# Kernel optimization log

Hardware: AMD Instinct MI355X
Metric: run time of the kernel (lower is better)

The kernel has to match this reference:

```python
import jax, jax.numpy as jnp
import numpy as np

D_MODEL, N_LEVELS, N_HEADS, N_POINTS = 256, 3, 8, 2
HEAD_DIM = D_MODEL // N_HEADS
SPATIAL_SHAPES = np.array([[100, 100], [50, 50], [25, 25]], dtype=np.int32)
LEN_IN = int((SPATIAL_SHAPES[:, 0] * SPATIAL_SHAPES[:, 1]).sum())  # 13125
BS, NQ = 16, 900


def setup_inputs() -> dict:
    key = jax.random.key(0)
    ks = jax.random.split(key, 12)
    s = 1.0 / np.sqrt(D_MODEL)
    return {
        "query": jax.random.normal(ks[0], (BS, NQ, N_LEVELS, D_MODEL), jnp.float32),
        "reference_points": jax.random.uniform(ks[1], (BS, NQ, N_LEVELS, 2), jnp.float32),
        "input_flatten": jax.random.normal(ks[2], (BS, LEN_IN, D_MODEL), jnp.float32),
        "input_spatial_shapes": jnp.asarray(SPATIAL_SHAPES),
        "W_value": jax.random.normal(ks[3], (D_MODEL, D_MODEL), jnp.float32) * s,
        "b_value": jnp.zeros((D_MODEL,), jnp.float32),
        "W_off": jax.random.normal(ks[4], (D_MODEL, N_HEADS * N_LEVELS * N_POINTS * 2), jnp.float32) * s * 0.1,
        "b_off": jax.random.normal(ks[5], (N_HEADS * N_LEVELS * N_POINTS * 2,), jnp.float32) * 0.5,
        "W_attn": jax.random.normal(ks[6], (D_MODEL, N_HEADS * N_LEVELS * N_POINTS), jnp.float32) * s,
        "b_attn": jnp.zeros((N_HEADS * N_LEVELS * N_POINTS,), jnp.float32),
        "W_out": jax.random.normal(ks[7], (D_MODEL, D_MODEL), jnp.float32) * s,
        "b_out": jnp.zeros((D_MODEL,), jnp.float32),
    }


def _bilinear_sample(v, loc, H, W):
    """v: (bs, nh, H*W, hd); loc in [0,1]: (bs, nh, N, 2). Zero-pad out of range."""
    hd = v.shape[-1]
    x = loc[..., 0] * W - 0.5
    y = loc[..., 1] * H - 0.5
    x0 = jnp.floor(x)
    y0 = jnp.floor(y)
    out = jnp.zeros(x.shape + (hd,), v.dtype)
    for dx in (0, 1):
        for dy in (0, 1):
            xi = x0 + dx
            yi = y0 + dy
            wgt = (1.0 - jnp.abs(x - xi)) * (1.0 - jnp.abs(y - yi))
            valid = (xi >= 0) & (xi <= W - 1) & (yi >= 0) & (yi <= H - 1)
            xi_c = jnp.clip(xi, 0, W - 1).astype(jnp.int32)
            yi_c = jnp.clip(yi, 0, H - 1).astype(jnp.int32)
            idx = yi_c * W + xi_c  # (bs, nh, N)
            idx = jnp.broadcast_to(idx[..., None], idx.shape + (hd,))
            g = jnp.take_along_axis(v, idx, axis=2)  # (bs, nh, N, hd)
            out = out + g * (wgt * valid.astype(wgt.dtype))[..., None]
    return out


def reference(query, reference_points, input_flatten, input_spatial_shapes,
              W_value, b_value, W_off, b_off, W_attn, b_attn, W_out, b_out):
    bs, nq, fl, _ = query.shape
    shapes = np.asarray(input_spatial_shapes)  # static pyramid shapes

    # value projection: (bs, Len, nh, hd)
    value = (input_flatten @ W_value + b_value).reshape(bs, -1, N_HEADS, HEAD_DIM)

    # sampling offsets: (bs, nq, fl, nh, nl, np, 2)
    offsets = (query @ W_off + b_off).reshape(bs, nq, fl, N_HEADS, N_LEVELS, N_POINTS, 2)
    # attention weights softmax over (nl*np): (bs, nq, fl, nh, nl, np)
    attn = (query @ W_attn + b_attn).reshape(bs, nq, fl, N_HEADS, N_LEVELS * N_POINTS)
    attn = jax.nn.softmax(attn, axis=-1).reshape(bs, nq, fl, N_HEADS, N_LEVELS, N_POINTS)

    # normalized sampling locations: ref + offset / (W_l, H_l)
    normalizer = jnp.asarray(shapes[:, ::-1], jnp.float32)  # (nl, 2) = (W, H)
    loc = reference_points[:, :, :, None, None, None, :] + offsets / normalizer[None, None, None, None, :, None, :]

    splits = np.cumsum([h * w for h, w in shapes])[:-1]
    value_list = jnp.split(value, splits, axis=1)

    out = jnp.zeros((bs, N_HEADS, nq, fl, HEAD_DIM), value.dtype)
    for lvl, (H, W) in enumerate(shapes):
        H, W = int(H), int(W)
        v = jnp.transpose(value_list[lvl], (0, 2, 1, 3))  # (bs, nh, H*W, hd)
        loc_l = jnp.transpose(loc[:, :, :, :, lvl], (0, 3, 1, 2, 4, 5))  # (bs, nh, nq, fl, np, 2)
        loc_flat = loc_l.reshape(bs, N_HEADS, nq * fl * N_POINTS, 2)
        sampled = _bilinear_sample(v, loc_flat, H, W).reshape(bs, N_HEADS, nq, fl, N_POINTS, HEAD_DIM)
        w = jnp.transpose(attn[:, :, :, :, lvl], (0, 3, 1, 2, 4))  # (bs, nh, nq, fl, np)
        out = out + jnp.einsum("bhqfpd,bhqfp->bhqfd", sampled, w)

    out = jnp.transpose(out, (0, 2, 3, 1, 4)).reshape(bs, nq, fl, D_MODEL)
    return out @ W_out + b_out
```

## Files before the change

kernel.cpp:

```cpp
#include <hip/hip_runtime.h>
#include <math.h>

#define D_MODEL   256
#define N_HEADS   8
#define HEAD_DIM  32
#define N_LEVELS  3
#define N_POINTS  2
#define BS        16
#define NQ        900
#define LEN_IN    13125
#define M_Q       (BS * NQ * N_LEVELS)
#define M_V       (BS * LEN_IN)
#define NCAT      144
#define NCATP     192

typedef _Float16 f16x8 __attribute__((ext_vector_type(8)));
typedef _Float16 f16x4 __attribute__((ext_vector_type(4)));
typedef float f32x4 __attribute__((ext_vector_type(4)));

__global__ __launch_bounds__(256) void convert_weight_kernel(
    const float* __restrict__ W, _Float16* __restrict__ Wth,
    _Float16* __restrict__ Wtl, int N, int Npad) {
  const int idx = blockIdx.x * 256 + threadIdx.x;
  if (idx >= Npad * 256) return;
  const int n = idx >> 8;
  const int k = idx & 255;
  const float v = (n < N) ? W[(size_t)k * N + n] : 0.0f;
  const _Float16 h = (_Float16)v;
  Wth[idx] = h;
  Wtl[idx] = (_Float16)(v - (float)h);
}

__global__ __launch_bounds__(256) void convert_cat_kernel(
    const float* __restrict__ Woff, const float* __restrict__ Wattn,
    const float* __restrict__ boff, const float* __restrict__ battn,
    _Float16* __restrict__ Wth, _Float16* __restrict__ Wtl,
    float* __restrict__ bcat) {
  const int idx = blockIdx.x * 256 + threadIdx.x;
  if (idx >= NCATP * 256) return;
  const int n = idx >> 8;
  const int k = idx & 255;
  float v = 0.0f;
  if (n < 96) v = Woff[(size_t)k * 96 + n];
  else if (n < NCAT) v = Wattn[(size_t)k * 48 + (n - 96)];
  const _Float16 h = (_Float16)v;
  Wth[idx] = h;
  Wtl[idx] = (_Float16)(v - (float)h);
  if (idx < NCAT) bcat[idx] = (idx < 96) ? boff[idx] : battn[idx - 96];
}

template <int FC>
__global__ __launch_bounds__(256) void gemm3_kernel(
    const float* __restrict__ A, const _Float16* __restrict__ Bth,
    const _Float16* __restrict__ Btl, const float* __restrict__ bias,
    float* __restrict__ C, int M, int N) {
  constexpr int K = 256;
  __shared__ _Float16 Ah[64 * 256];
  __shared__ _Float16 Al[64 * 256];

  const int tid = threadIdx.x;
  const int wid = tid >> 6;
  const int lane = tid & 63;
  const int bm = blockIdx.x * 64;
  const int rsel = lane & 15;
  const int khi = (lane >> 4) * 8;

  char* AhB = (char*)Ah;
  char* AlB = (char*)Al;

#pragma unroll
  for (int it = 0; it < 16; ++it) {
    const int idx = it * 1024 + tid * 4;
    const int row = idx >> 8;
    const int col = idx & 255;
    float4 v = make_float4(0.f, 0.f, 0.f, 0.f);
    if (bm + row < M)
      v = *reinterpret_cast<const float4*>(&A[(size_t)(bm + row) * K + col]);
    f16x4 h, l;
    h[0] = (_Float16)v.x; l[0] = (_Float16)(v.x - (float)h[0]);
    h[1] = (_Float16)v.y; l[1] = (_Float16)(v.y - (float)h[1]);
    h[2] = (_Float16)v.z; l[2] = (_Float16)(v.z - (float)h[2]);
    h[3] = (_Float16)v.w; l[3] = (_Float16)(v.w - (float)h[3]);
    const int byt = row * 512 + ((col * 2) ^ ((row & 7) << 4));
    *reinterpret_cast<f16x4*>(AhB + byt) = h;
    *reinterpret_cast<f16x4*>(AlB + byt) = l;
  }

  const _Float16* bhp = Bth + (size_t)(wid * FC * 16 + rsel) * K + khi;
  const _Float16* blp = Btl + (size_t)(wid * FC * 16 + rsel) * K + khi;

  f32x4 acc[4][FC];
#pragma unroll
  for (int fr = 0; fr < 4; ++fr)
#pragma unroll
    for (int fc = 0; fc < FC; ++fc) acc[fr][fc] = (f32x4)0.0f;

  f16x8 bh[FC], bl[FC];
#pragma unroll
  for (int fc = 0; fc < FC; ++fc) {
    bh[fc] = *reinterpret_cast<const f16x8*>(bhp + (size_t)fc * 16 * K);
    bl[fc] = *reinterpret_cast<const f16x8*>(blp + (size_t)fc * 16 * K);
  }

  __syncthreads();

  const int swzx = (rsel & 7) << 4;

#pragma unroll
  for (int s = 0; s < 8; ++s) {
    f16x8 nbh[FC], nbl[FC];
    if (s < 7) {
#pragma unroll
      for (int fc = 0; fc < FC; ++fc) {
        nbh[fc] = *reinterpret_cast<const f16x8*>(
            bhp + (size_t)fc * 16 * K + (s + 1) * 32);
        nbl[fc] = *reinterpret_cast<const f16x8*>(
            blp + (size_t)fc * 16 * K + (s + 1) * 32);
      }
    }
    f16x8 afh[4], afl[4];
#pragma unroll
    for (int fr = 0; fr < 4; ++fr) {
      const int row = fr * 16 + rsel;
      const int byt = row * 512 + (((s * 32 + khi) * 2) ^ swzx);
      afh[fr] = *reinterpret_cast<const f16x8*>(AhB + byt);
      afl[fr] = *reinterpret_cast<const f16x8*>(AlB + byt);
    }
#pragma unroll
    for (int fr = 0; fr < 4; ++fr)
#pragma unroll
      for (int fc = 0; fc < FC; ++fc) {
        acc[fr][fc] = __builtin_amdgcn_mfma_f32_16x16x32_f16(
            afh[fr], bh[fc], acc[fr][fc], 0, 0, 0);
        acc[fr][fc] = __builtin_amdgcn_mfma_f32_16x16x32_f16(
            afh[fr], bl[fc], acc[fr][fc], 0, 0, 0);
        acc[fr][fc] = __builtin_amdgcn_mfma_f32_16x16x32_f16(
            afl[fr], bh[fc], acc[fr][fc], 0, 0, 0);
      }
    if (s < 7) {
#pragma unroll
      for (int fc = 0; fc < FC; ++fc) { bh[fc] = nbh[fc]; bl[fc] = nbl[fc]; }
    }
  }

  float bs_[FC];
#pragma unroll
  for (int fc = 0; fc < FC; ++fc) {
    const int col = wid * FC * 16 + fc * 16 + rsel;
    bs_[fc] = (col < N) ? bias[col] : 0.0f;
  }
#pragma unroll
  for (int fr = 0; fr < 4; ++fr)
#pragma unroll
    for (int i = 0; i < 4; ++i) {
      const int row = bm + fr * 16 + (lane >> 4) * 4 + i;
      if (row >= M) continue;
#pragma unroll
      for (int fc = 0; fc < FC; ++fc) {
        const int col = wid * FC * 16 + fc * 16 + rsel;
        if (col < N) C[(size_t)row * N + col] = acc[fr][fc][i] + bs_[fc];
      }
    }
}

__global__ __launch_bounds__(256) void sample2_kernel(
    const float* __restrict__ value, const float* __restrict__ refpts,
    const float* __restrict__ offs_attn, float* __restrict__ out_mid) {
  __shared__ int4   s_off[144];
  __shared__ float4 s_w[144];

  const int bq = blockIdx.x;
  const int b = bq / NQ;
  const int tid = threadIdx.x;

  if (tid < 144) {
    const int fl = tid / 48;
    const int rem = tid - fl * 48;
    const int h = rem / 6;
    const int j = rem - h * 6;
    const int l = j >> 1;

    const int LVL_W[3] = {100, 50, 25};
    const int LVL_BASE[3] = {0, 10000, 12500};
    const int W = LVL_W[l];
    const int base = LVL_BASE[l];
    const float fW = (float)W, fH = (float)W;

    const int row = bq * 3 + fl;
    const float* oa = offs_attn + (size_t)row * NCAT;

    float aw[6];
    float mx = -INFINITY;
#pragma unroll
    for (int jj = 0; jj < 6; ++jj) {
      aw[jj] = oa[96 + h * 6 + jj];
      mx = fmaxf(mx, aw[jj]);
    }
    float ssum = 0.f;
#pragma unroll
    for (int jj = 0; jj < 6; ++jj) ssum += expf(aw[jj] - mx);
    const float wa = expf(aw[j] - mx) / ssum;

    const float rx = refpts[(size_t)row * 2 + 0];
    const float ry = refpts[(size_t)row * 2 + 1];
    const float ox = oa[h * 12 + j * 2 + 0];
    const float oy = oa[h * 12 + j * 2 + 1];
    const float x = (rx + ox / fW) * fW - 0.5f;
    const float y = (ry + oy / fH) * fH - 0.5f;
    const float x0 = floorf(x);
    const float y0 = floorf(y);

    int offv[4];
    float wv[4];
#pragma unroll
    for (int dy = 0; dy < 2; ++dy)
#pragma unroll
      for (int dx = 0; dx < 2; ++dx) {
        const float xi = x0 + (float)dx;
        const float yi = y0 + (float)dy;
        const float wgt = (1.0f - fabsf(x - xi)) * (1.0f - fabsf(y - yi));
        const bool valid = (xi >= 0.f) && (xi <= fW - 1.f) &&
                           (yi >= 0.f) && (yi <= fH - 1.f);
        const int xic = (int)fminf(fmaxf(xi, 0.f), fW - 1.f);
        const int yic = (int)fminf(fmaxf(yi, 0.f), fH - 1.f);
        const int pos = base + yic * W + xic;
        offv[dy * 2 + dx] = pos * 1024;
        wv[dy * 2 + dx] = valid ? wgt * wa : 0.0f;
      }
    s_off[tid] = make_int4(offv[0], offv[1], offv[2], offv[3]);
    s_w[tid] = make_float4(wv[0], wv[1], wv[2], wv[3]);
  }
  __syncthreads();

  const int h = tid >> 5;
  const int d = tid & 31;
  const char* vb = (const char*)value +
                   ((size_t)b * LEN_IN * 256 + h * 32 + d) * 4;

#pragma unroll
  for (int fl = 0; fl < 3; ++fl) {
    float acc = 0.f;
#pragma unroll
    for (int j = 0; j < 6; ++j) {
      const int rec = fl * 48 + h * 6 + j;
      const int4 o = s_off[rec];
      const float4 w = s_w[rec];
      acc = fmaf(w.x, *(const float*)(vb + o.x), acc);
      acc = fmaf(w.y, *(const float*)(vb + o.y), acc);
      acc = fmaf(w.z, *(const float*)(vb + o.z), acc);
      acc = fmaf(w.w, *(const float*)(vb + o.w), acc);
    }
    out_mid[((size_t)bq * 3 + fl) * 256 + tid] = acc;
  }
}

extern "C" void kernel_launch(void* const* d_in, const int* in_sizes, int n_in,
                              void* d_out, int out_size, void* d_ws,
                              size_t ws_size, hipStream_t stream) {
  const float* query   = (const float*)d_in[0];
  const float* refpts  = (const float*)d_in[1];
  const float* in_flat = (const float*)d_in[2];
  const float* W_value = (const float*)d_in[4];
  const float* b_value = (const float*)d_in[5];
  const float* W_off   = (const float*)d_in[6];
  const float* b_off   = (const float*)d_in[7];
  const float* W_attn  = (const float*)d_in[8];
  const float* b_attn  = (const float*)d_in[9];
  const float* W_out   = (const float*)d_in[10];
  const float* b_out   = (const float*)d_in[11];
  float* out = (float*)d_out;

  char* ws = (char*)d_ws;
  float* value     = (float*)ws; ws += (size_t)M_V * 256 * sizeof(float);
  float* out_mid   = (float*)ws; ws += (size_t)M_Q * 256 * sizeof(float);
  float* offs_attn = (float*)ws; ws += (size_t)M_Q * NCAT * sizeof(float);
  _Float16* Wvh = (_Float16*)ws; ws += 256 * 256 * sizeof(_Float16);
  _Float16* Wvl = (_Float16*)ws; ws += 256 * 256 * sizeof(_Float16);
  _Float16* Woh = (_Float16*)ws; ws += 256 * 256 * sizeof(_Float16);
  _Float16* Wol = (_Float16*)ws; ws += 256 * 256 * sizeof(_Float16);
  _Float16* Wch = (_Float16*)ws; ws += NCATP * 256 * sizeof(_Float16);
  _Float16* Wcl = (_Float16*)ws; ws += NCATP * 256 * sizeof(_Float16);
  float* bcat   = (float*)ws;    ws += 256 * sizeof(float);

  const dim3 blk(256);

  convert_weight_kernel<<<dim3(256), blk, 0, stream>>>(W_value, Wvh, Wvl, 256, 256);
  convert_weight_kernel<<<dim3(256), blk, 0, stream>>>(W_out,   Woh, Wol, 256, 256);
  convert_cat_kernel<<<dim3(NCATP), blk, 0, stream>>>(W_off, W_attn, b_off, b_attn,
                                                      Wch, Wcl, bcat);

  gemm3_kernel<4><<<dim3((M_V + 63) / 64), blk, 0, stream>>>(
      in_flat, Wvh, Wvl, b_value, value, M_V, 256);

  gemm3_kernel<3><<<dim3((M_Q + 63) / 64), blk, 0, stream>>>(
      query, Wch, Wcl, bcat, offs_attn, M_Q, NCAT);

  sample2_kernel<<<dim3(BS * NQ), blk, 0, stream>>>(value, refpts, offs_attn,
                                                    out_mid);

  gemm3_kernel<4><<<dim3((M_Q + 63) / 64), blk, 0, stream>>>(
      out_mid, Woh, Wol, b_out, out, M_Q, 256);
}
```

Baseline: 853.9 us.

## Split GEMM into column-half tiles with K-chunked LDS and packed B fragments

```diff
diff --git a/kernel.cpp b/kernel.cpp
--- a/kernel.cpp
+++ b/kernel.cpp
@@ -12,29 +12,30 @@
 #define M_Q       (BS * NQ * N_LEVELS)
 #define M_V       (BS * LEN_IN)
 #define NCAT      144
-#define NCATP     192
+#define NCATP     256
 
 typedef _Float16 f16x8 __attribute__((ext_vector_type(8)));
 typedef _Float16 f16x4 __attribute__((ext_vector_type(4)));
 typedef float f32x4 __attribute__((ext_vector_type(4)));
 
 __global__ __launch_bounds__(256) void convert_weight_kernel(
-    const float* __restrict__ W, _Float16* __restrict__ Wth,
-    _Float16* __restrict__ Wtl, int N, int Npad) {
+    const float* __restrict__ W, _Float16* __restrict__ Wph,
+    _Float16* __restrict__ Wpl, int N, int Npad) {
   const int idx = blockIdx.x * 256 + threadIdx.x;
   if (idx >= Npad * 256) return;
   const int n = idx >> 8;
   const int k = idx & 255;
   const float v = (n < N) ? W[(size_t)k * N + n] : 0.0f;
   const _Float16 h = (_Float16)v;
-  Wth[idx] = h;
-  Wtl[idx] = (_Float16)(v - (float)h);
+  const int dst = (((n >> 4) * 32) + (k >> 3)) * 128 + (n & 15) * 8 + (k & 7);
+  Wph[dst] = h;
+  Wpl[dst] = (_Float16)(v - (float)h);
 }
 
 __global__ __launch_bounds__(256) void convert_cat_kernel(
     const float* __restrict__ Woff, const float* __restrict__ Wattn,
     const float* __restrict__ boff, const float* __restrict__ battn,
-    _Float16* __restrict__ Wth, _Float16* __restrict__ Wtl,
+    _Float16* __restrict__ Wph, _Float16* __restrict__ Wpl,
     float* __restrict__ bcat) {
   const int idx = blockIdx.x * 256 + threadIdx.x;
   if (idx >= NCATP * 256) return;
@@ -44,50 +45,41 @@
   if (n < 96) v = Woff[(size_t)k * 96 + n];
   else if (n < NCAT) v = Wattn[(size_t)k * 48 + (n - 96)];
   const _Float16 h = (_Float16)v;
-  Wth[idx] = h;
-  Wtl[idx] = (_Float16)(v - (float)h);
+  const int dst = (((n >> 4) * 32) + (k >> 3)) * 128 + (n & 15) * 8 + (k & 7);
+  Wph[dst] = h;
+  Wpl[dst] = (_Float16)(v - (float)h);
   if (idx < NCAT) bcat[idx] = (idx < 96) ? boff[idx] : battn[idx - 96];
 }
 
-template <int FC>
-__global__ __launch_bounds__(256) void gemm3_kernel(
-    const float* __restrict__ A, const _Float16* __restrict__ Bth,
-    const _Float16* __restrict__ Btl, const float* __restrict__ bias,
+template <int FC, int TAG>
+__global__ __launch_bounds__(256, 4) void gemm4_kernel(
+    const float* __restrict__ A, const _Float16* __restrict__ Bph,
+    const _Float16* __restrict__ Bpl, const float* __restrict__ bias,
     float* __restrict__ C, int M, int N) {
   constexpr int K = 256;
-  __shared__ _Float16 Ah[64 * 256];
-  __shared__ _Float16 Al[64 * 256];
+  __shared__ _Float16 AhL[64 * 128];
+  __shared__ _Float16 AlL[64 * 128];
 
   const int tid = threadIdx.x;
   const int wid = tid >> 6;
   const int lane = tid & 63;
-  const int bm = blockIdx.x * 64;
+  const int bx = blockIdx.x;
+  const int bm = blockIdx.y * 64;
   const int rsel = lane & 15;
-  const int khi = (lane >> 4) * 8;
-
-  char* AhB = (char*)Ah;
-  char* AlB = (char*)Al;
-
-#pragma unroll
-  for (int it = 0; it < 16; ++it) {
-    const int idx = it * 1024 + tid * 4;
-    const int row = idx >> 8;
-    const int col = idx & 255;
-    float4 v = make_float4(0.f, 0.f, 0.f, 0.f);
-    if (bm + row < M)
-      v = *reinterpret_cast<const float4*>(&A[(size_t)(bm + row) * K + col]);
-    f16x4 h, l;
-    h[0] = (_Float16)v.x; l[0] = (_Float16)(v.x - (float)h[0]);
-    h[1] = (_Float16)v.y; l[1] = (_Float16)(v.y - (float)h[1]);
-    h[2] = (_Float16)v.z; l[2] = (_Float16)(v.z - (float)h[2]);
-    h[3] = (_Float16)v.w; l[3] = (_Float16)(v.w - (float)h[3]);
-    const int byt = row * 512 + ((col * 2) ^ ((row & 7) << 4));
-    *reinterpret_cast<f16x4*>(AhB + byt) = h;
-    *reinterpret_cast<f16x4*>(AlB + byt) = l;
-  }
-
-  const _Float16* bhp = Bth + (size_t)(wid * FC * 16 + rsel) * K + khi;
-  const _Float16* blp = Btl + (size_t)(wid * FC * 16 + rsel) * K + khi;
+  const int q = (lane >> 4) & 3;
+  const int swzx = (rsel & 7) << 4;
+
+  char* AhB = (char*)AhL;
+  char* AlB = (char*)AlL;
+
+  const _Float16* bph[FC];
+  const _Float16* bpl[FC];
+#pragma unroll
+  for (int fc = 0; fc < FC; ++fc) {
+    const int g = bx * 8 + wid * 2 + fc;
+    bph[fc] = Bph + (size_t)g * 4096 + lane * 8;
+    bpl[fc] = Bpl + (size_t)g * 4096 + lane * 8;
+  }
 
   f32x4 acc[4][FC];
 #pragma unroll
@@ -95,58 +87,73 @@
 #pragma unroll
     for (int fc = 0; fc < FC; ++fc) acc[fr][fc] = (f32x4)0.0f;
 
-  f16x8 bh[FC], bl[FC];
+#pragma unroll
+  for (int c = 0; c < 2; ++c) {
+    if (c == 1) __syncthreads();
+#pragma unroll
+    for (int it = 0; it < 8; ++it) {
+      const int i = it * 1024 + tid * 4;
+      const int row = i >> 7;
+      const int col = i & 127;
+      float4 v = make_float4(0.f, 0.f, 0.f, 0.f);
+      if (bm + row < M)
+        v = *reinterpret_cast<const float4*>(
+            &A[(size_t)(bm + row) * K + c * 128 + col]);
+      f16x4 h, l;
+      h[0] = (_Float16)v.x; l[0] = (_Float16)(v.x - (float)h[0]);
+      h[1] = (_Float16)v.y; l[1] = (_Float16)(v.y - (float)h[1]);
+      h[2] = (_Float16)v.z; l[2] = (_Float16)(v.z - (float)h[2]);
+      h[3] = (_Float16)v.w; l[3] = (_Float16)(v.w - (float)h[3]);
+      const int byt = row * 256 + ((col * 2) ^ ((row & 7) << 4));
+      *reinterpret_cast<f16x4*>(AhB + byt) = h;
+      *reinterpret_cast<f16x4*>(AlB + byt) = l;
+    }
+    __syncthreads();
+
+#pragma unroll
+    for (int sl = 0; sl < 4; ++sl) {
+      const int s = c * 4 + sl;
+      f16x8 bh[FC], bl[FC], afh[4], afl[4];
+#pragma unroll
+      for (int fc = 0; fc < FC; ++fc) {
+        bh[fc] = *reinterpret_cast<const f16x8*>(bph[fc] + s * 512);
+        bl[fc] = *reinterpret_cast<const f16x8*>(bpl[fc] + s * 512);
+      }
+#pragma unroll
+      for (int fr = 0; fr < 4; ++fr) {
+        const int row = fr * 16 + rsel;
+        const int byt = row * 256 + ((sl * 64 + q * 16) ^ swzx);
+        afh[fr] = *reinterpret_cast<const f16x8*>(AhB + byt);
+        afl[fr] = *reinterpret_cast<const f16x8*>(AlB + byt);
+      }
+      __builtin_amdgcn_s_setprio(1);
+#pragma unroll
+      for (int fr = 0; fr < 4; ++fr)
+#pragma unroll
+        for (int fc = 0; fc < FC; ++fc)
+          acc[fr][fc] = __builtin_amdgcn_mfma_f32_16x16x32_f16(
+              afh[fr], bh[fc], acc[fr][fc], 0, 0, 0);
+#pragma unroll
+      for (int fr = 0; fr < 4; ++fr)
+#pragma unroll
+        for (int fc = 0; fc < FC; ++fc)
+          acc[fr][fc] = __builtin_amdgcn_mfma_f32_16x16x32_f16(
+              afh[fr], bl[fc], acc[fr][fc], 0, 0, 0);
+#pragma unroll
+      for (int fr = 0; fr < 4; ++fr)
+#pragma unroll
+        for (int fc = 0; fc < FC; ++fc)
+          acc[fr][fc] = __builtin_amdgcn_mfma_f32_16x16x32_f16(
+              afl[fr], bh[fc], acc[fr][fc], 0, 0, 0);
+      __builtin_amdgcn_s_setprio(0);
+    }
+  }
+
+  const int colbase = bx * 128 + wid * 32;
+  float bs_[FC];
 #pragma unroll
   for (int fc = 0; fc < FC; ++fc) {
-    bh[fc] = *reinterpret_cast<const f16x8*>(bhp + (size_t)fc * 16 * K);
-    bl[fc] = *reinterpret_cast<const f16x8*>(blp + (size_t)fc * 16 * K);
-  }
-
-  __syncthreads();
-
-  const int swzx = (rsel & 7) << 4;
-
-#pragma unroll
-  for (int s = 0; s < 8; ++s) {
-    f16x8 nbh[FC], nbl[FC];
-    if (s < 7) {
-#pragma unroll
-      for (int fc = 0; fc < FC; ++fc) {
-        nbh[fc] = *reinterpret_cast<const f16x8*>(
-            bhp + (size_t)fc * 16 * K + (s + 1) * 32);
-        nbl[fc] = *reinterpret_cast<const f16x8*>(
-            blp + (size_t)fc * 16 * K + (s + 1) * 32);
-      }
-    }
-    f16x8 afh[4], afl[4];
-#pragma unroll
-    for (int fr = 0; fr < 4; ++fr) {
-      const int row = fr * 16 + rsel;
-      const int byt = row * 512 + (((s * 32 + khi) * 2) ^ swzx);
-      afh[fr] = *reinterpret_cast<const f16x8*>(AhB + byt);
-      afl[fr] = *reinterpret_cast<const f16x8*>(AlB + byt);
-    }
-#pragma unroll
-    for (int fr = 0; fr < 4; ++fr)
-#pragma unroll
-      for (int fc = 0; fc < FC; ++fc) {
-        acc[fr][fc] = __builtin_amdgcn_mfma_f32_16x16x32_f16(
-            afh[fr], bh[fc], acc[fr][fc], 0, 0, 0);
-        acc[fr][fc] = __builtin_amdgcn_mfma_f32_16x16x32_f16(
-            afh[fr], bl[fc], acc[fr][fc], 0, 0, 0);
-        acc[fr][fc] = __builtin_amdgcn_mfma_f32_16x16x32_f16(
-            afl[fr], bh[fc], acc[fr][fc], 0, 0, 0);
-      }
-    if (s < 7) {
-#pragma unroll
-      for (int fc = 0; fc < FC; ++fc) { bh[fc] = nbh[fc]; bl[fc] = nbl[fc]; }
-    }
-  }
-
-  float bs_[FC];
-#pragma unroll
-  for (int fc = 0; fc < FC; ++fc) {
-    const int col = wid * FC * 16 + fc * 16 + rsel;
+    const int col = colbase + fc * 16 + rsel;
     bs_[fc] = (col < N) ? bias[col] : 0.0f;
   }
 #pragma unroll
@@ -157,7 +164,7 @@
       if (row >= M) continue;
 #pragma unroll
       for (int fc = 0; fc < FC; ++fc) {
-        const int col = wid * FC * 16 + fc * 16 + rsel;
+        const int col = colbase + fc * 16 + rsel;
         if (col < N) C[(size_t)row * N + col] = acc[fr][fc][i] + bs_[fc];
       }
     }
@@ -289,15 +296,15 @@
   convert_cat_kernel<<<dim3(NCATP), blk, 0, stream>>>(W_off, W_attn, b_off, b_attn,
                                                       Wch, Wcl, bcat);
 
-  gemm3_kernel<4><<<dim3((M_V + 63) / 64), blk, 0, stream>>>(
+  gemm4_kernel<2, 1><<<dim3(2, (M_V + 63) / 64), blk, 0, stream>>>(
       in_flat, Wvh, Wvl, b_value, value, M_V, 256);
 
-  gemm3_kernel<3><<<dim3((M_Q + 63) / 64), blk, 0, stream>>>(
+  gemm4_kernel<2, 2><<<dim3(2, (M_Q + 63) / 64), blk, 0, stream>>>(
       query, Wch, Wcl, bcat, offs_attn, M_Q, NCAT);
 
   sample2_kernel<<<dim3(BS * NQ), blk, 0, stream>>>(value, refpts, offs_attn,
                                                     out_mid);
 
-  gemm3_kernel<4><<<dim3((M_Q + 63) / 64), blk, 0, stream>>>(
+  gemm4_kernel<2, 3><<<dim3(2, (M_Q + 63) / 64), blk, 0, stream>>>(
       out_mid, Woh, Wol, b_out, out, M_Q, 256);
 }
```

Result: faster. 777.8 us (-8.9%).
